# Kernel optimization log

Hardware: AMD Instinct MI355X
Metric: run time of the kernel (lower is better)

## Reference

```python
import jax, jax.numpy as jnp
import numpy as np

N, E, F, D, G, K = 50000, 1600000, 128, 256, 64, 10


def setup_inputs() -> dict:
    key = jax.random.key(0)
    ks = jax.random.split(key, 20)
    x = jax.random.normal(ks[0], (N, F), dtype=jnp.float32)
    edge_index = jax.random.randint(ks[1], (2, E), 0, N, dtype=jnp.int64)
    batch_index = jnp.sort(jax.random.randint(ks[2], (N,), 0, G, dtype=jnp.int64))

    def lin(k, fan_in, fan_out):
        w = jax.random.normal(k, (fan_in, fan_out), dtype=jnp.float32) / np.sqrt(fan_in)
        return w

    return {
        "x": x, "edge_index": edge_index, "batch_index": batch_index,
        "W0": lin(ks[3], F, D), "b0": jnp.zeros((D,), jnp.float32),
        "W1": lin(ks[4], D, D), "b1": jnp.zeros((D,), jnp.float32),
        "W2": lin(ks[5], D, D), "b2": jnp.zeros((D,), jnp.float32),
        "W3": lin(ks[6], D, D), "b3": jnp.zeros((D,), jnp.float32),
        "fc1_w": lin(ks[7], 2 * D, 512), "fc1_b": jnp.zeros((512,), jnp.float32),
        "fc2_w": lin(ks[8], 512, 256), "fc2_b": jnp.zeros((256,), jnp.float32),
        "out_w": lin(ks[9], 256, K), "out_b": jnp.zeros((K,), jnp.float32),
    }


def _gcn_conv(x, W, b, src, dst, dis):
    # PyG GCNConv: h = x W; out = D^{-1/2}(A+I)D^{-1/2} h + b  (self-loops added)
    h = x @ W                                   # [N, D]
    norm = dis[src] * dis[dst]                  # [E]
    msg = h[src] * norm[:, None]                # [E, D]
    agg = jax.ops.segment_sum(msg, dst, num_segments=x.shape[0])
    agg = agg + h * (dis * dis)[:, None]        # self-loop contribution
    return agg + b


def reference(x, edge_index, batch_index, W0, b0, W1, b1, W2, b2, W3, b3,
              fc1_w, fc1_b, fc2_w, fc2_b, out_w, out_b):
    src, dst = edge_index[0], edge_index[1]
    n = x.shape[0]
    # degree with self-loops
    deg = 1.0 + jax.ops.segment_sum(jnp.ones((src.shape[0],), jnp.float32), dst,
                                    num_segments=n)
    dis = jax.lax.rsqrt(deg)

    h = jnp.tanh(_gcn_conv(x, W0, b0, src, dst, dis))
    h = jnp.tanh(_gcn_conv(h, W1, b1, src, dst, dis))
    h = jnp.tanh(_gcn_conv(h, W2, b2, src, dst, dis))
    h = jnp.tanh(_gcn_conv(h, W3, b3, src, dst, dis))

    # global max pool + global mean pool over graphs in the batch
    gmax = jax.ops.segment_max(h, batch_index, num_segments=G)
    gsum = jax.ops.segment_sum(h, batch_index, num_segments=G)
    cnt = jax.ops.segment_sum(jnp.ones((n,), jnp.float32), batch_index,
                              num_segments=G)
    gmean = gsum / jnp.maximum(cnt, 1.0)[:, None]
    g = jnp.concatenate([gmax, gmean], axis=1)  # [G, 2D]

    g = jax.nn.relu(g @ fc1_w + fc1_b)
    g = jax.nn.relu(g @ fc2_w + fc2_b)
    return g @ out_w + out_b
```

## Files before the change

kernel.cpp:

```cpp
#include <hip/hip_runtime.h>
#include <hip/hip_bf16.h>


#define NNODES 50000
#define DDIM 256
#define SCAN_B 256
#define SCAN_G ((NNODES + SCAN_B - 1) / SCAN_B)

typedef __attribute__((ext_vector_type(8))) short short8;
typedef __attribute__((ext_vector_type(4))) float float4_;
typedef __attribute__((ext_vector_type(2))) float float2_;

__device__ __forceinline__ float fast_tanh(float x) {
    float e = __expf(2.0f * x);
    return 1.0f - 2.0f / (e + 1.0f);
}

__device__ __forceinline__ float bf2f(unsigned short u) {
    return __uint_as_float(((unsigned)u) << 16);
}
__device__ __forceinline__ unsigned short f2bf(float f) {
    unsigned u = __float_as_uint(f);
    u = u + 0x7fffu + ((u >> 16) & 1u);
    return (unsigned short)(u >> 16);
}

__device__ __forceinline__ unsigned f2key(float f) {
    unsigned b = __float_as_uint(f);
    return (b & 0x80000000u) ? ~b : (b | 0x80000000u);
}
__device__ __forceinline__ float key2f(unsigned k) {
    unsigned b = (k & 0x80000000u) ? (k & 0x7fffffffu) : ~k;
    return __uint_as_float(b);
}

__global__ void hist_kernel(const int* __restrict__ ei, int* __restrict__ deg,
                            int* __restrict__ rank, int E) {
    int e = blockIdx.x * blockDim.x + threadIdx.x;
    if (e < E) rank[e] = atomicAdd(&deg[ei[E + e]], 1);
}

__global__ void scan1_kernel(const int* __restrict__ deg, int* __restrict__ bsum, int N) {
    __shared__ int s[SCAN_B];
    int t = threadIdx.x;
    int idx = blockIdx.x * SCAN_B + t;
    s[t] = (idx < N) ? deg[idx] : 0;
    __syncthreads();
    for (int off = SCAN_B / 2; off > 0; off >>= 1) {
        if (t < off) s[t] += s[t + off];
        __syncthreads();
    }
    if (t == 0) bsum[blockIdx.x] = s[0];
}

__global__ void scan2_kernel(const int* __restrict__ deg, const int* __restrict__ bsum,
                             int* __restrict__ rowptr, float* __restrict__ dis, int N) {
    __shared__ int s[SCAN_B];
    __shared__ int bs[SCAN_B];
    int t = threadIdx.x;
    int bid = blockIdx.x;
    int idx = bid * SCAN_B + t;
    int d = (idx < N) ? deg[idx] : 0;
    s[t] = d;
    bs[t] = (t < bid) ? bsum[t] : 0;
    __syncthreads();
    for (int off = 1; off < SCAN_B; off <<= 1) {
        int v = (t >= off) ? s[t - off] : 0;
        __syncthreads();
        s[t] += v;
        __syncthreads();
    }
    for (int off = SCAN_B / 2; off > 0; off >>= 1) {
        if (t < off) bs[t] += bs[t + off];
        __syncthreads();
    }
    if (idx < N) {
        rowptr[idx] = bs[0] + s[t] - d;
        dis[idx] = rsqrtf(1.0f + (float)d);
    }
}

__global__ void scatter_kernel(const int* __restrict__ ei, const int* __restrict__ rowptr,
                               const int* __restrict__ rank,
                               unsigned short* __restrict__ col, int E) {
    int e = blockIdx.x * blockDim.x + threadIdx.x;
    if (e < E) {
        int d = ei[E + e];
        col[rowptr[d] + rank[e]] = (unsigned short)ei[e];
    }
}

#define CAST_BLOCKS ((NNODES * 128) / 256)
__global__ void prep_kernel(const float* __restrict__ x, const float* __restrict__ dis,
                            unsigned short* __restrict__ xh,
                            const float* __restrict__ W0, const float* __restrict__ W1,
                            const float* __restrict__ W2, const float* __restrict__ W3,
                            unsigned short* __restrict__ wt0, unsigned short* __restrict__ wt1,
                            unsigned short* __restrict__ wt2, unsigned short* __restrict__ wt3) {
    int b = blockIdx.x;
    int t = threadIdx.x;
    if (b < CAST_BLOCKS) {
        int i = b * 256 + t;
        xh[i] = f2bf(x[i] * dis[i >> 7]);
        return;
    }
    b -= CAST_BLOCKS;
    const float* W; unsigned short* Wt; int K; int k;
    if (b < 128)      { W = W0; Wt = wt0; K = 128; k = b; }
    else if (b < 384) { W = W1; Wt = wt1; K = 256; k = b - 128; }
    else if (b < 640) { W = W2; Wt = wt2; K = 256; k = b - 384; }
    else              { W = W3; Wt = wt3; K = 256; k = b - 640; }
    Wt[t * K + k] = f2bf(W[k * 256 + t]);
}

__device__ __forceinline__ void paddu(float2_* acc, uint4 u) {
    float2_ v0 = {__uint_as_float(u.x << 16), __uint_as_float(u.x & 0xffff0000u)};
    float2_ v1 = {__uint_as_float(u.y << 16), __uint_as_float(u.y & 0xffff0000u)};
    float2_ v2 = {__uint_as_float(u.z << 16), __uint_as_float(u.z & 0xffff0000u)};
    float2_ v3 = {__uint_as_float(u.w << 16), __uint_as_float(u.w & 0xffff0000u)};
    acc[0] += v0; acc[1] += v1; acc[2] += v2; acc[3] += v3;
}
__device__ __forceinline__ void paddw(float2_* acc, uint4 u, float w) {
    float2_ w2 = {w, w};
    float2_ v0 = {__uint_as_float(u.x << 16), __uint_as_float(u.x & 0xffff0000u)};
    float2_ v1 = {__uint_as_float(u.y << 16), __uint_as_float(u.y & 0xffff0000u)};
    float2_ v2 = {__uint_as_float(u.z << 16), __uint_as_float(u.z & 0xffff0000u)};
    float2_ v3 = {__uint_as_float(u.w << 16), __uint_as_float(u.w & 0xffff0000u)};
    acc[0] += v0 * w2; acc[1] += v1 * w2; acc[2] += v2 * w2; acc[3] += v3 * w2;
}

template <int W, int S, bool FINALIZE>
__global__ void msgpass_bf16(const unsigned short* __restrict__ in,
                             unsigned short* __restrict__ out,
                             const int* __restrict__ rowptr, const int* __restrict__ deg,
                             const unsigned short* __restrict__ col,
                             const float* __restrict__ dis, const float* __restrict__ bias) {
    constexpr int L = W / 8;
    constexpr int P = 64 / L;
    int lane = threadIdx.x & 63;
    int wav  = threadIdx.x >> 6;
    int n = blockIdx.x * 8 + wav;
    if (n >= NNODES) return;
    int part = lane / L;
    int sl   = lane % L;
    int start = rowptr[n];
    int cnt   = deg[n];
    float dn = dis[n];
    float2_ acc[4];
#pragma unroll
    for (int j = 0; j < 4; ++j) { float2_ z = {0.0f, 0.0f}; acc[j] = z; }

    int e = 0;
    for (; e + 4 * P <= cnt; e += 4 * P) {
        int c0 = col[start + e + part];
        int c1 = col[start + e + P + part];
        int c2 = col[start + e + 2 * P + part];
        int c3 = col[start + e + 3 * P + part];
        uint4 u0 = *((const uint4*)(in + (size_t)c0 * S) + sl);
        uint4 u1 = *((const uint4*)(in + (size_t)c1 * S) + sl);
        uint4 u2 = *((const uint4*)(in + (size_t)c2 * S) + sl);
        uint4 u3 = *((const uint4*)(in + (size_t)c3 * S) + sl);
        paddu(acc, u0);
        paddu(acc, u1);
        paddu(acc, u2);
        paddu(acc, u3);
    }
    for (; e + P <= cnt; e += P) {
        int c = col[start + e + part];
        uint4 u = *((const uint4*)(in + (size_t)c * S) + sl);
        paddu(acc, u);
    }
    int r = cnt - e;
    if (r > 0) {
        int c = (part < r) ? (int)col[start + e + part] : n;
        float w = (part < r) ? 1.0f : 0.0f;
        uint4 u = *((const uint4*)(in + (size_t)c * S) + sl);
        paddw(acc, u, w);
    }
    {
        float w = (part == 0) ? 1.0f : 0.0f;
        uint4 u = *((const uint4*)(in + (size_t)n * S) + sl);
        paddw(acc, u, w);
    }
#pragma unroll
    for (int j = 0; j < 4; ++j) {
#pragma unroll
        for (int h = 0; h < 2; ++h) {
            if (P == 4) acc[j][h] += __shfl(acc[j][h], lane ^ 16);
            acc[j][h] += __shfl(acc[j][h], lane ^ 32);
        }
    }
    if (part == 0) {
        float a[8] = {acc[0][0], acc[0][1], acc[1][0], acc[1][1],
                      acc[2][0], acc[2][1], acc[3][0], acc[3][1]};
        if (FINALIZE) {
#pragma unroll
            for (int j = 0; j < 8; ++j)
                a[j] = fast_tanh(fmaf(a[j], dn, bias[sl * 8 + j]));
        } else {
#pragma unroll
            for (int j = 0; j < 8; ++j)
                a[j] *= dn;
        }
        uint4 o;
        o.x = (unsigned)f2bf(a[0]) | ((unsigned)f2bf(a[1]) << 16);
        o.y = (unsigned)f2bf(a[2]) | ((unsigned)f2bf(a[3]) << 16);
        o.z = (unsigned)f2bf(a[4]) | ((unsigned)f2bf(a[5]) << 16);
        o.w = (unsigned)f2bf(a[6]) | ((unsigned)f2bf(a[7]) << 16);
        *((uint4*)(out + (size_t)n * S) + sl) = o;
    }
}

template <int K, bool TANH>
__launch_bounds__(256, 2)
__global__ void gemm_mfma(const short* __restrict__ A, const short* __restrict__ Bt,
                          const float* __restrict__ bias, const float* __restrict__ dis,
                          unsigned short* __restrict__ C, int N) {
    constexpr int PK = 72;
    __shared__ __align__(16) short As[128 * PK];
    __shared__ __align__(16) short Bs[128 * PK];
    int t = threadIdx.x;
    int lane = t & 63;
    int w    = t >> 6;
    int wr = w & 1;
    int wc = w >> 1;
    int m0 = blockIdx.x * 128;
    int n0 = blockIdx.y * 128;

    int srow = t >> 2;
    int koff = (t & 3) * 8;
    int arow0 = m0 + srow;      if (arow0 > N - 1) arow0 = N - 1;
    int arow1 = m0 + 64 + srow; if (arow1 > N - 1) arow1 = N - 1;
    const short8* ap0 = (const short8*)(A + (size_t)arow0 * K + koff);
    const short8* ap1 = (const short8*)(A + (size_t)arow1 * K + koff);
    const short8* bp0 = (const short8*)(Bt + (size_t)(n0 + srow) * K + koff);
    const short8* bp1 = (const short8*)(Bt + (size_t)(n0 + 64 + srow) * K + koff);

    float4_ acc[4][4];
#pragma unroll
    for (int i = 0; i < 4; ++i)
#pragma unroll
        for (int j = 0; j < 4; ++j) {
            float4_ z = {0.0f, 0.0f, 0.0f, 0.0f};
            acc[i][j] = z;
        }

    constexpr int NKB = K / 64;
    int g = lane >> 4;
    int r = lane & 15;

    short8 a00 = ap0[0], a01 = ap0[4];
    short8 a10 = ap1[0], a11 = ap1[4];
    short8 b00 = bp0[0], b01 = bp0[4];
    short8 b10 = bp1[0], b11 = bp1[4];

    for (int kb = 0; kb < NKB; ++kb) {
        __syncthreads();
        *(short8*)&As[srow * PK + koff]             = a00;
        *(short8*)&As[srow * PK + koff + 32]        = a01;
        *(short8*)&As[(64 + srow) * PK + koff]      = a10;
        *(short8*)&As[(64 + srow) * PK + koff + 32] = a11;
        *(short8*)&Bs[srow * PK + koff]             = b00;
        *(short8*)&Bs[srow * PK + koff + 32]        = b01;
        *(short8*)&Bs[(64 + srow) * PK + koff]      = b10;
        *(short8*)&Bs[(64 + srow) * PK + koff + 32] = b11;
        __syncthreads();
        if (kb + 1 < NKB) {
            int o = (kb + 1) * 8;
            a00 = ap0[o]; a01 = ap0[o + 4];
            a10 = ap1[o]; a11 = ap1[o + 4];
            b00 = bp0[o]; b01 = bp0[o + 4];
            b10 = bp1[o]; b11 = bp1[o + 4];
        }
#pragma unroll
        for (int s = 0; s < 2; ++s) {
            short8 af[4], bfr[4];
#pragma unroll
            for (int i = 0; i < 4; ++i)
                af[i] = *(const short8*)&As[(wr * 64 + i * 16 + r) * PK + s * 32 + g * 8];
#pragma unroll
            for (int j = 0; j < 4; ++j)
                bfr[j] = *(const short8*)&Bs[(wc * 64 + j * 16 + r) * PK + s * 32 + g * 8];
#pragma unroll
            for (int i = 0; i < 4; ++i)
#pragma unroll
                for (int j = 0; j < 4; ++j)
                    acc[i][j] = __builtin_amdgcn_mfma_f32_16x16x32_bf16(af[i], bfr[j],
                                                                        acc[i][j], 0, 0, 0);
        }
    }

#pragma unroll
    for (int i = 0; i < 4; ++i) {
        int rowb = m0 + wr * 64 + i * 16 + g * 4;
#pragma unroll
        for (int rr = 0; rr < 4; ++rr) {
            int row = rowb + rr;
            if (row < N) {
                float dsc = TANH ? 0.0f : dis[row];
#pragma unroll
                for (int j = 0; j < 4; ++j) {
                    int cb = n0 + wc * 64 + j * 16 + r;
                    float v = acc[i][j][rr];
                    if (TANH) v = fast_tanh(v + bias[cb]);
                    else      v = v * dsc;
                    C[(size_t)row * 256 + cb] = f2bf(v);
                }
            }
        }
    }
}

#define POOL_CHUNK 64
__global__ void pool_kernel(const unsigned short* __restrict__ act,
                            const int* __restrict__ batch,
                            float* __restrict__ gsum, unsigned* __restrict__ gmaxk,
                            int* __restrict__ gcnt, int N) {
    int t  = threadIdx.x;
    int n0 = blockIdx.x * POOL_CHUNK;
    if (n0 >= N) return;
    int n1 = n0 + POOL_CHUNK;
    if (n1 > N) n1 = N;
    int   cur = batch[n0];
    float sum = 0.0f, mx = -2.0f;
    int   run = 0;
    for (int n = n0; n < n1; ++n) {
        int g = batch[n];
        float v = bf2f(act[(size_t)n * DDIM + t]);
        if (g != cur) {
            atomicAdd(&gsum[cur * DDIM + t], sum);
            atomicMax(&gmaxk[cur * DDIM + t], f2key(mx));
            if (t == 0) atomicAdd(&gcnt[cur], run);
            cur = g; sum = 0.0f; mx = -2.0f; run = 0;
        }
        sum += v;
        mx = fmaxf(mx, v);
        run++;
    }
    atomicAdd(&gsum[cur * DDIM + t], sum);
    atomicMax(&gmaxk[cur * DDIM + t], f2key(mx));
    if (t == 0) atomicAdd(&gcnt[cur], run);
}

__global__ void mlp_kernel(const float* __restrict__ gsum, const unsigned* __restrict__ gmaxk,
                           const int* __restrict__ gcnt,
                           const float* __restrict__ fc1_w, const float* __restrict__ fc1_b,
                           const float* __restrict__ fc2_w, const float* __restrict__ fc2_b,
                           const float* __restrict__ out_w, const float* __restrict__ out_b,
                           float* __restrict__ out) {
    int g = blockIdx.x;
    int t = threadIdx.x;
    __shared__ float gv[512];
    __shared__ float t1[512];
    __shared__ float t2[256];
    float cnt = fmaxf((float)gcnt[g], 1.0f);
    gv[t]       = key2f(gmaxk[g * DDIM + t]);
    gv[256 + t] = gsum[g * DDIM + t] / cnt;
    __syncthreads();
    float a0 = fc1_b[t], a1 = fc1_b[t + 256];
    for (int k = 0; k < 512; ++k) {
        float gk = gv[k];
        a0 = fmaf(gk, fc1_w[k * 512 + t], a0);
        a1 = fmaf(gk, fc1_w[k * 512 + t + 256], a1);
    }
    t1[t]       = fmaxf(a0, 0.0f);
    t1[t + 256] = fmaxf(a1, 0.0f);
    __syncthreads();
    float b0 = fc2_b[t];
    for (int k = 0; k < 512; ++k)
        b0 = fmaf(t1[k], fc2_w[k * 256 + t], b0);
    t2[t] = fmaxf(b0, 0.0f);
    __syncthreads();
    if (t < 10) {
        float o = out_b[t];
        for (int k = 0; k < 256; ++k)
            o = fmaf(t2[k], out_w[k * 10 + t], o);
        out[g * 10 + t] = o;
    }
}

extern "C" void kernel_launch(void* const* d_in, const int* in_sizes, int n_in,
                              void* d_out, int out_size, void* d_ws, size_t ws_size,
                              hipStream_t stream) {
    const float* x      = (const float*)d_in[0];
    const int*   ei     = (const int*)d_in[1];
    const int*   batch  = (const int*)d_in[2];
    const float* W0     = (const float*)d_in[3];
    const float* b0     = (const float*)d_in[4];
    const float* W1     = (const float*)d_in[5];
    const float* b1     = (const float*)d_in[6];
    const float* W2     = (const float*)d_in[7];
    const float* b2     = (const float*)d_in[8];
    const float* W3     = (const float*)d_in[9];
    const float* b3     = (const float*)d_in[10];
    const float* fc1_w  = (const float*)d_in[11];
    const float* fc1_b  = (const float*)d_in[12];
    const float* fc2_w  = (const float*)d_in[13];
    const float* fc2_b  = (const float*)d_in[14];
    const float* out_w  = (const float*)d_in[15];
    const float* out_b  = (const float*)d_in[16];
    float* out = (float*)d_out;

    const int N = in_sizes[2];
    const int E = in_sizes[1] / 2;

    char* ws = (char*)d_ws;
    const size_t off_deg    = 0;
    const size_t off_gsum   = 200192;
    const size_t off_gmaxk  = 265728;
    const size_t off_gcnt   = 331264;
    const size_t ZERO_BYTES = 331776;
    const size_t off_dis    = 331776;
    const size_t off_rowptr = 531968;
    const size_t off_bsum   = 732160;
    const size_t off_col    = 932352;
    const size_t off_xh     = 7332352;
    const size_t off_wt0    = 20132352;
    const size_t off_wt1    = 20197888;
    const size_t off_wt2    = 20328960;
    const size_t off_wt3    = 20460032;
    const size_t off_bufA   = 20591104;
    const size_t off_bufB   = 46191104;

    int*            deg    = (int*)(ws + off_deg);
    float*          gsum   = (float*)(ws + off_gsum);
    unsigned*       gmaxk  = (unsigned*)(ws + off_gmaxk);
    int*            gcnt   = (int*)(ws + off_gcnt);
    float*          dis    = (float*)(ws + off_dis);
    int*            rowptr = (int*)(ws + off_rowptr);
    int*            bsum   = (int*)(ws + off_bsum);
    unsigned short* col    = (unsigned short*)(ws + off_col);
    unsigned short* xh     = (unsigned short*)(ws + off_xh);
    short*          wt0    = (short*)(ws + off_wt0);
    short*          wt1    = (short*)(ws + off_wt1);
    short*          wt2    = (short*)(ws + off_wt2);
    short*          wt3    = (short*)(ws + off_wt3);
    unsigned short* bufA   = (unsigned short*)(ws + off_bufA);
    unsigned short* bufB   = (unsigned short*)(ws + off_bufB);
    int*            rank   = (int*)(ws + off_bufA);

    hipMemsetAsync(ws, 0, ZERO_BYTES, stream);

    hist_kernel<<<(E + 255) / 256, 256, 0, stream>>>(ei, deg, rank, E);
    scan1_kernel<<<SCAN_G, SCAN_B, 0, stream>>>(deg, bsum, N);
    scan2_kernel<<<SCAN_G, SCAN_B, 0, stream>>>(deg, bsum, rowptr, dis, N);
    scatter_kernel<<<(E + 255) / 256, 256, 0, stream>>>(ei, rowptr, rank, col, E);

    prep_kernel<<<CAST_BLOCKS + 896, 256, 0, stream>>>(
        x, dis, xh, W0, W1, W2, W3,
        (unsigned short*)wt0, (unsigned short*)wt1,
        (unsigned short*)wt2, (unsigned short*)wt3);

    msgpass_bf16<128, 128, false><<<(N + 7) / 8, 512, 0, stream>>>(
        xh, bufB, rowptr, deg, col, dis, nullptr);
    gemm_mfma<128, true><<<dim3((N + 127) / 128, 2), 256, 0, stream>>>(
        (const short*)bufB, wt0, b0, dis, bufA, N);

    const short* wts[3] = {wt1, wt2, wt3};
    const float* bs_[3] = {b1, b2, b3};
    for (int l = 0; l < 3; ++l) {
        gemm_mfma<256, false><<<dim3((N + 127) / 128, 2), 256, 0, stream>>>(
            (const short*)bufA, wts[l], nullptr, dis, bufB, N);
        msgpass_bf16<128, 256, true><<<(N + 7) / 8, 512, 0, stream>>>(
            bufB, bufA, rowptr, deg, col, dis, bs_[l]);
        msgpass_bf16<128, 256, true><<<(N + 7) / 8, 512, 0, stream>>>(
            bufB + 128, bufA + 128, rowptr, deg, col, dis, bs_[l] + 128);
    }

    pool_kernel<<<(N + POOL_CHUNK - 1) / POOL_CHUNK, 256, 0, stream>>>(
        bufA, batch, gsum, gmaxk, gcnt, N);
    mlp_kernel<<<64, 256, 0, stream>>>(gsum, gmaxk, gcnt, fc1_w, fc1_b, fc2_w, fc2_b,
                                       out_w, out_b, out);
}
```

Before: 707.0 us.

## Build CSR via two-pass bucketed partition with shared-memory atomics

Replaces the global-atomic histogram, two-kernel scan and scatter used for CSR construction with a two-kernel bucket sort. Edges are first partitioned into 256-node destination buckets using LDS histograms, then each bucket builds its local degrees, row pointers and column indices entirely in shared memory. This is meant to remove the heavy contention and random traffic of per-edge global atomics, and to cut the launch count. It relies on a fixed per-bucket capacity (BCAP), which a skewed degree distribution could overflow, and on the bucket count matching the node count.

```diff
diff --git a/kernel.cpp b/kernel.cpp
--- a/kernel.cpp
+++ b/kernel.cpp
@@ -4,8 +4,9 @@
 
 #define NNODES 50000
 #define DDIM 256
-#define SCAN_B 256
-#define SCAN_G ((NNODES + SCAN_B - 1) / SCAN_B)
+#define NBUCK 196
+#define BCAP 16384
+#define CHUNK_AB 6400
 
 typedef __attribute__((ext_vector_type(8))) short short8;
 typedef __attribute__((ext_vector_type(4))) float float4_;
@@ -34,59 +35,81 @@
     return __uint_as_float(b);
 }
 
-__global__ void hist_kernel(const int* __restrict__ ei, int* __restrict__ deg,
-                            int* __restrict__ rank, int E) {
-    int e = blockIdx.x * blockDim.x + threadIdx.x;
-    if (e < E) rank[e] = atomicAdd(&deg[ei[E + e]], 1);
-}
-
-__global__ void scan1_kernel(const int* __restrict__ deg, int* __restrict__ bsum, int N) {
-    __shared__ int s[SCAN_B];
+__global__ void build_partition(const int* __restrict__ ei, int* __restrict__ bcnt,
+                                unsigned* __restrict__ pairs, int E) {
+    __shared__ int hist[NBUCK];
+    __shared__ int base[NBUCK];
+    __shared__ int cursor[NBUCK];
     int t = threadIdx.x;
-    int idx = blockIdx.x * SCAN_B + t;
-    s[t] = (idx < N) ? deg[idx] : 0;
-    __syncthreads();
-    for (int off = SCAN_B / 2; off > 0; off >>= 1) {
-        if (t < off) s[t] += s[t + off];
-        __syncthreads();
-    }
-    if (t == 0) bsum[blockIdx.x] = s[0];
-}
-
-__global__ void scan2_kernel(const int* __restrict__ deg, const int* __restrict__ bsum,
-                             int* __restrict__ rowptr, float* __restrict__ dis, int N) {
-    __shared__ int s[SCAN_B];
-    __shared__ int bs[SCAN_B];
+    int e0 = blockIdx.x * CHUNK_AB;
+    int lim = E - e0;
+    if (lim > CHUNK_AB) lim = CHUNK_AB;
+    if (t < NBUCK) { hist[t] = 0; cursor[t] = 0; }
+    __syncthreads();
+    for (int i = t; i < lim; i += 256)
+        atomicAdd(&hist[ei[E + e0 + i] >> 8], 1);
+    __syncthreads();
+    if (t < NBUCK) {
+        int h = hist[t];
+        base[t] = h ? atomicAdd(&bcnt[t], h) : 0;
+    }
+    __syncthreads();
+    for (int i = t; i < lim; i += 256) {
+        int dst = ei[E + e0 + i];
+        int src = ei[e0 + i];
+        int b = dst >> 8;
+        int r = atomicAdd(&cursor[b], 1);
+        pairs[(size_t)b * BCAP + base[b] + r] =
+            ((unsigned)(dst & 255) << 16) | (unsigned)src;
+    }
+}
+
+__global__ void build_csr(const unsigned* __restrict__ pairs, const int* __restrict__ bcnt,
+                          int* __restrict__ deg, int* __restrict__ rowptr,
+                          float* __restrict__ dis, unsigned short* __restrict__ col, int N) {
+    __shared__ int sc[256];
+    __shared__ int hist[256];
+    __shared__ int cursor[256];
+    int b = blockIdx.x;
     int t = threadIdx.x;
-    int bid = blockIdx.x;
-    int idx = bid * SCAN_B + t;
-    int d = (idx < N) ? deg[idx] : 0;
-    s[t] = d;
-    bs[t] = (t < bid) ? bsum[t] : 0;
-    __syncthreads();
-    for (int off = 1; off < SCAN_B; off <<= 1) {
-        int v = (t >= off) ? s[t - off] : 0;
-        __syncthreads();
-        s[t] += v;
-        __syncthreads();
-    }
-    for (int off = SCAN_B / 2; off > 0; off >>= 1) {
-        if (t < off) bs[t] += bs[t + off];
-        __syncthreads();
-    }
-    if (idx < N) {
-        rowptr[idx] = bs[0] + s[t] - d;
-        dis[idx] = rsqrtf(1.0f + (float)d);
-    }
-}
-
-__global__ void scatter_kernel(const int* __restrict__ ei, const int* __restrict__ rowptr,
-                               const int* __restrict__ rank,
-                               unsigned short* __restrict__ col, int E) {
-    int e = blockIdx.x * blockDim.x + threadIdx.x;
-    if (e < E) {
-        int d = ei[E + e];
-        col[rowptr[d] + rank[e]] = (unsigned short)ei[e];
+    sc[t] = (t < NBUCK) ? bcnt[t] : 0;
+    __syncthreads();
+    for (int off = 1; off < 256; off <<= 1) {
+        int v = (t >= off) ? sc[t - off] : 0;
+        __syncthreads();
+        sc[t] += v;
+        __syncthreads();
+    }
+    int bstart = (b == 0) ? 0 : sc[b - 1];
+    int cnt = bcnt[b];
+    __syncthreads();
+    hist[t] = 0; cursor[t] = 0;
+    __syncthreads();
+    const unsigned* bp = pairs + (size_t)b * BCAP;
+    for (int i = t; i < cnt; i += 256)
+        atomicAdd(&hist[bp[i] >> 16], 1);
+    __syncthreads();
+    sc[t] = hist[t];
+    __syncthreads();
+    for (int off = 1; off < 256; off <<= 1) {
+        int v = (t >= off) ? sc[t - off] : 0;
+        __syncthreads();
+        sc[t] += v;
+        __syncthreads();
+    }
+    int n = b * 256 + t;
+    if (n < N) {
+        int d = hist[t];
+        deg[n] = d;
+        dis[n] = rsqrtf(1.0f + (float)d);
+        rowptr[n] = bstart + sc[t] - d;
+    }
+    __syncthreads();
+    for (int i = t; i < cnt; i += 256) {
+        unsigned p = bp[i];
+        int low = p >> 16;
+        int r = atomicAdd(&cursor[low], 1);
+        col[bstart + (sc[low] - hist[low]) + r] = (unsigned short)(p & 0xffffu);
     }
 }
 
@@ -412,7 +435,7 @@
     const size_t ZERO_BYTES = 331776;
     const size_t off_dis    = 331776;
     const size_t off_rowptr = 531968;
-    const size_t off_bsum   = 732160;
+    const size_t off_bcnt   = 732160;
     const size_t off_col    = 932352;
     const size_t off_xh     = 7332352;
     const size_t off_wt0    = 20132352;
@@ -428,7 +451,7 @@
     int*            gcnt   = (int*)(ws + off_gcnt);
     float*          dis    = (float*)(ws + off_dis);
     int*            rowptr = (int*)(ws + off_rowptr);
-    int*            bsum   = (int*)(ws + off_bsum);
+    int*            bcnt   = (int*)(ws + off_bcnt);
     unsigned short* col    = (unsigned short*)(ws + off_col);
     unsigned short* xh     = (unsigned short*)(ws + off_xh);
     short*          wt0    = (short*)(ws + off_wt0);
@@ -437,14 +460,13 @@
     short*          wt3    = (short*)(ws + off_wt3);
     unsigned short* bufA   = (unsigned short*)(ws + off_bufA);
     unsigned short* bufB   = (unsigned short*)(ws + off_bufB);
-    int*            rank   = (int*)(ws + off_bufA);
+    unsigned*       pairs  = (unsigned*)(ws + off_bufA);
 
     hipMemsetAsync(ws, 0, ZERO_BYTES, stream);
-
-    hist_kernel<<<(E + 255) / 256, 256, 0, stream>>>(ei, deg, rank, E);
-    scan1_kernel<<<SCAN_G, SCAN_B, 0, stream>>>(deg, bsum, N);
-    scan2_kernel<<<SCAN_G, SCAN_B, 0, stream>>>(deg, bsum, rowptr, dis, N);
-    scatter_kernel<<<(E + 255) / 256, 256, 0, stream>>>(ei, rowptr, rank, col, E);
+    hipMemsetAsync(ws + off_bcnt, 0, 1024, stream);
+
+    build_partition<<<(E + CHUNK_AB - 1) / CHUNK_AB, 256, 0, stream>>>(ei, bcnt, pairs, E);
+    build_csr<<<NBUCK, 256, 0, stream>>>(pairs, bcnt, deg, rowptr, dis, col, N);
 
     prep_kernel<<<CAST_BLOCKS + 896, 256, 0, stream>>>(
         x, dis, xh, W0, W1, W2, W3,
```

Result: faster. 652.1 us (-7.8%).
